# Kernel tuning notes

Measured on AMD Instinct MI355X. Metric: run time of the kernel, lower is better.

Reference implementation:

```python
import jax, jax.numpy as jnp
import numpy as np

TEMPERATURE = 8.0  # sqrt(head_dim=64)
_MASKING_VALUE = -1e30  # float32 branch of the original module


def setup_inputs() -> dict:
    key = jax.random.key(0)
    kq, kk, kv = jax.random.split(key, 3)
    B, H, S, D = 2, 12, 2048, 64
    q = jax.random.normal(kq, (B, H, S, D), dtype=jnp.float32)
    k = jax.random.normal(kk, (B, H, S, D), dtype=jnp.float32)
    v = jax.random.normal(kv, (B, H, S, D), dtype=jnp.float32)
    # causal mask, broadcastable over batch and heads; mask==0 -> masked
    mask = jnp.tril(jnp.ones((S, S), dtype=jnp.bool_))[None, None, :, :]
    return {"q": q, "k": k, "v": v, "mask": mask}


def reference(q, k, v, mask):
    # attn = (q / temperature) @ k^T  -> [B,H,S,S]
    scores = jnp.einsum("bhqd,bhkd->bhqk", q / TEMPERATURE, k)
    scores = jnp.where(mask, scores, _MASKING_VALUE)
    attn = jax.nn.softmax(scores, axis=-1)  # dropout in eval mode (identity)
    output = jnp.einsum("bhqk,bhkd->bhqd", attn, v)
    return (output, attn)
```

## Files before the change

kernel.cpp:

```cpp
#include <hip/hip_runtime.h>
#include <hip/hip_bf16.h>
#include <stdint.h>

#define SS 2048
#define DD 64
#define NHEAD 24
#define TK 64
#define NKT 32

typedef __attribute__((ext_vector_type(8))) short short8;
typedef __attribute__((ext_vector_type(4))) short short4v;
typedef __attribute__((ext_vector_type(4))) float f32x4;

#define QSCALE 0.18033688011112042f
#define MLOG   46.166241308446828f

#if __has_builtin(__builtin_amdgcn_exp2f)
#define EXP2(x) __builtin_amdgcn_exp2f(x)
#else
#define EXP2(x) exp2f(x)
#endif

__device__ __forceinline__ unsigned short f2bf(float x) {
  union { float f; unsigned u; } a; a.f = x;
  unsigned r = a.u + 0x7FFFu + ((a.u >> 16) & 1u);
  return (unsigned short)(r >> 16);
}

__device__ __forceinline__ void stage16(const unsigned char* g, unsigned char* l) {
  __builtin_amdgcn_global_load_lds(
      (const __attribute__((address_space(1))) unsigned int*)g,
      (__attribute__((address_space(3))) unsigned int*)l, 16, 0, 0);
}

__global__ __launch_bounds__(256) void prep_kernel(
    const float* __restrict__ q, const float* __restrict__ k,
    const float* __restrict__ v, unsigned short* __restrict__ qb,
    unsigned char* __restrict__ kb, unsigned char* __restrict__ vtb) {
  const int head = blockIdx.x >> 5;
  const int t64 = blockIdx.x & 31;
  const int tid = threadIdx.x;
  const int c4 = tid & 15;
  const size_t inbase = ((size_t)head * SS + (size_t)t64 * 64) * DD;
  const f32x4* qsrc = (const f32x4*)(q + inbase);
  const f32x4* ksrc = (const f32x4*)(k + inbase);
  const f32x4* vsrc = (const f32x4*)(v + inbase);
  unsigned short* qdst = qb + inbase;
  unsigned char* ktile = kb + ((size_t)(head * NKT + t64) << 13);
  unsigned char* vtile = vtb + ((size_t)(head * NKT + t64) << 13);
#pragma unroll
  for (int j = 0; j < 4; ++j) {
    const int row = (tid >> 4) + 16 * j;
    f32x4 xq = qsrc[row * 16 + c4];
    short4v hq;
    hq.x = (short)f2bf(xq.x * QSCALE); hq.y = (short)f2bf(xq.y * QSCALE);
    hq.z = (short)f2bf(xq.z * QSCALE); hq.w = (short)f2bf(xq.w * QSCALE);
    *(short4v*)(qdst + row * 64 + c4 * 4) = hq;

    f32x4 xk = ksrc[row * 16 + c4];
    short4v hk;
    hk.x = (short)f2bf(xk.x); hk.y = (short)f2bf(xk.y);
    hk.z = (short)f2bf(xk.z); hk.w = (short)f2bf(xk.w);
    const int chunk = c4 >> 1, half = c4 & 1;
    *(short4v*)(ktile + row * 128 + ((chunk ^ (row & 7)) << 4) + half * 8) = hk;

    f32x4 xv = vsrc[row * 16 + c4];
    float vals[4] = {xv.x, xv.y, xv.z, xv.w};
#pragma unroll
    for (int e = 0; e < 4; ++e) {
      const int d = c4 * 4 + e;
      *(unsigned short*)(vtile + d * 128 + (((row >> 3) ^ (d & 7)) << 4) +
                         (row & 7) * 2) = f2bf(vals[e]);
    }
  }
}

__global__ __launch_bounds__(256) void sdpa_kernel(
    const unsigned short* __restrict__ qb, const unsigned char* __restrict__ kb,
    const unsigned char* __restrict__ vtb, float* __restrict__ out,
    float* __restrict__ attn) {
  __shared__ unsigned char lds[32768];

  const int bid = blockIdx.x;
  const int xcd = bid & 7;
  const int seq = bid >> 3;
  const int head = xcd * 3 + (seq >> 5);
  const int qt = seq & 31;
  const int q0 = qt * TK;

  const int tid = threadIdx.x;
  const int w = tid >> 6;
  const int l = tid & 63;
  const int lhi = l >> 4;
  const int llo = l & 15;
  const int qrl = 16 * w + llo;

  const unsigned short* qh = qb + (size_t)head * SS * DD;
  const unsigned char* kh = kb + ((size_t)(head * NKT) << 13);
  const unsigned char* vh = vtb + ((size_t)(head * NKT) << 13);
  float* oh = out + (size_t)head * SS * DD;
  float* ah = attn + (size_t)head * SS * SS;
  float* ah_row = ah + (size_t)(q0 + qrl) * SS;

  short8 qf0 = *(const short8*)(qh + (size_t)(q0 + qrl) * DD + lhi * 8);
  short8 qf1 = *(const short8*)(qh + (size_t)(q0 + qrl) * DD + lhi * 8 + 32);

  float lsum = 0.f;
  stage16(kh + tid * 16, lds + tid * 16);
  stage16(kh + 4096 + tid * 16, lds + 4096 + tid * 16);
  __syncthreads();
  int b = 0;
  for (int kt = 0; kt <= qt; ++kt) {
    if (kt < qt) {
      const unsigned char* src = kh + ((size_t)(kt + 1) << 13);
      unsigned char* dst = lds + (b ^ 1) * 8192;
      stage16(src + tid * 16, dst + tid * 16);
      stage16(src + 4096 + tid * 16, dst + 4096 + tid * 16);
    }
    const unsigned char* kbuf = lds + b * 8192;
    const bool diag = (kt == qt);
#pragma unroll
    for (int c = 0; c < 4; ++c) {
      const int br = 16 * c + llo;
      short8 kf0 = *(const short8*)(kbuf + br * 128 + ((lhi ^ (br & 7)) << 4));
      short8 kf1 = *(const short8*)(kbuf + br * 128 + (((lhi + 4) ^ (br & 7)) << 4));
      f32x4 acc = {0.f, 0.f, 0.f, 0.f};
      acc = __builtin_amdgcn_mfma_f32_16x16x32_bf16(kf0, qf0, acc, 0, 0, 0);
      acc = __builtin_amdgcn_mfma_f32_16x16x32_bf16(kf1, qf1, acc, 0, 0, 0);
#pragma unroll
      for (int r = 0; r < 4; ++r) {
        float sv = acc[r];
        if (diag && (16 * c + 4 * lhi + r > qrl)) sv = -INFINITY;
        lsum += EXP2(sv - MLOG);
      }
    }
    __syncthreads();
    b ^= 1;
  }
  lsum += __shfl_xor(lsum, 16);
  lsum += __shfl_xor(lsum, 32);
  const float linv = 1.0f / lsum;

  f32x4 o[4];
#pragma unroll
  for (int c = 0; c < 4; ++c) o[c] = (f32x4){0.f, 0.f, 0.f, 0.f};

  unsigned sv[8];
  int k0p = 0;

  b = 0;
  stage16(kh + tid * 16, lds + tid * 16);
  stage16(kh + 4096 + tid * 16, lds + 4096 + tid * 16);
  stage16(vh + tid * 16, lds + 16384 + tid * 16);
  stage16(vh + 4096 + tid * 16, lds + 16384 + 4096 + tid * 16);
  __syncthreads();

  const int i0 = ((((2 * lhi)) & 3) * 16 + llo) * 4;
  const int i1 = ((((2 * lhi) + 1) & 3) * 16 + llo) * 4;

  for (int kt = 0; kt <= qt; ++kt) {
    if (kt > 0) {
#pragma unroll
      for (int c = 0; c < 4; ++c) {
        f32x4 fo;
        fo.x = __uint_as_float(sv[2 * c] << 16);
        fo.y = __uint_as_float(sv[2 * c] & 0xFFFF0000u);
        fo.z = __uint_as_float(sv[2 * c + 1] << 16);
        fo.w = __uint_as_float(sv[2 * c + 1] & 0xFFFF0000u);
        __builtin_nontemporal_store(fo, (f32x4*)(ah_row + k0p + 16 * c + 4 * lhi));
      }
    }
    if (kt < qt) {
      const unsigned char* ksrc = kh + ((size_t)(kt + 1) << 13);
      const unsigned char* vsrc = vh + ((size_t)(kt + 1) << 13);
      unsigned char* kdst = lds + (b ^ 1) * 8192;
      unsigned char* vdst = lds + 16384 + (b ^ 1) * 8192;
      stage16(ksrc + tid * 16, kdst + tid * 16);
      stage16(ksrc + 4096 + tid * 16, kdst + 4096 + tid * 16);
      stage16(vsrc + tid * 16, vdst + tid * 16);
      stage16(vsrc + 4096 + tid * 16, vdst + 4096 + tid * 16);
    }
    const unsigned char* kbuf = lds + b * 8192;
    const unsigned char* vbuf = lds + 16384 + b * 8192;
    const bool diag = (kt == qt);

    unsigned pk[8];
#pragma unroll
    for (int c = 0; c < 4; ++c) {
      const int br = 16 * c + llo;
      short8 kf0 = *(const short8*)(kbuf + br * 128 + ((lhi ^ (br & 7)) << 4));
      short8 kf1 = *(const short8*)(kbuf + br * 128 + (((lhi + 4) ^ (br & 7)) << 4));
      f32x4 acc = {0.f, 0.f, 0.f, 0.f};
      acc = __builtin_amdgcn_mfma_f32_16x16x32_bf16(kf0, qf0, acc, 0, 0, 0);
      acc = __builtin_amdgcn_mfma_f32_16x16x32_bf16(kf1, qf1, acc, 0, 0, 0);
      float p[4];
#pragma unroll
      for (int r = 0; r < 4; ++r) {
        float s = acc[r];
        if (diag && (16 * c + 4 * lhi + r > qrl)) s = -INFINITY;
        p[r] = EXP2(s - MLOG) * linv;
      }
      pk[2 * c] = ((unsigned)f2bf(p[1]) << 16) | f2bf(p[0]);
      pk[2 * c + 1] = ((unsigned)f2bf(p[3]) << 16) | f2bf(p[2]);
    }

    union U { int i[4]; short8 v; } fa0, fa1;
#pragma unroll
    for (int jb = 0; jb < 2; ++jb) {
      int a0 = __builtin_amdgcn_ds_bpermute(i0, (int)pk[0 + jb]);
      int b0 = __builtin_amdgcn_ds_bpermute(i0, (int)pk[2 + jb]);
      fa0.i[jb] = (lhi < 2) ? a0 : b0;
      int a1 = __builtin_amdgcn_ds_bpermute(i1, (int)pk[0 + jb]);
      int b1 = __builtin_amdgcn_ds_bpermute(i1, (int)pk[2 + jb]);
      fa0.i[2 + jb] = (lhi < 2) ? a1 : b1;
      int c0 = __builtin_amdgcn_ds_bpermute(i0, (int)pk[4 + jb]);
      int d0 = __builtin_amdgcn_ds_bpermute(i0, (int)pk[6 + jb]);
      fa1.i[jb] = (lhi < 2) ? c0 : d0;
      int c1 = __builtin_amdgcn_ds_bpermute(i1, (int)pk[4 + jb]);
      int d1 = __builtin_amdgcn_ds_bpermute(i1, (int)pk[6 + jb]);
      fa1.i[2 + jb] = (lhi < 2) ? c1 : d1;
    }

#pragma unroll
    for (int c = 0; c < 4; ++c) {
      const int vr = 16 * c + llo;
      short8 vb0 = *(const short8*)(vbuf + vr * 128 + ((lhi ^ (vr & 7)) << 4));
      short8 vb1 = *(const short8*)(vbuf + vr * 128 + (((lhi + 4) ^ (vr & 7)) << 4));
      o[c] = __builtin_amdgcn_mfma_f32_16x16x32_bf16(fa0.v, vb0, o[c], 0, 0, 0);
      o[c] = __builtin_amdgcn_mfma_f32_16x16x32_bf16(fa1.v, vb1, o[c], 0, 0, 0);
    }

#pragma unroll
    for (int t = 0; t < 8; ++t) sv[t] = pk[t];
    k0p = kt * TK;
    __syncthreads();
    b ^= 1;
  }
#pragma unroll
  for (int c = 0; c < 4; ++c) {
    f32x4 fo;
    fo.x = __uint_as_float(sv[2 * c] << 16);
    fo.y = __uint_as_float(sv[2 * c] & 0xFFFF0000u);
    fo.z = __uint_as_float(sv[2 * c + 1] << 16);
    fo.w = __uint_as_float(sv[2 * c + 1] & 0xFFFF0000u);
    __builtin_nontemporal_store(fo, (f32x4*)(ah_row + k0p + 16 * c + 4 * lhi));
  }

  {
    const int zc = (qt + 1) * TK;
#pragma unroll
    for (int j = 0; j < 4; ++j) {
      int row = q0 + 16 * w + 4 * j + lhi;
      f32x4* dst = (f32x4*)(ah + (size_t)row * SS);
      f32x4 z = {0.f, 0.f, 0.f, 0.f};
      for (int c = (zc >> 2) + llo; c < (SS >> 2); c += 16)
        __builtin_nontemporal_store(z, dst + c);
    }
  }

#pragma unroll
  for (int c = 0; c < 4; ++c)
#pragma unroll
    for (int r = 0; r < 4; ++r) {
      int qrow = q0 + 16 * w + 4 * lhi + r;
      oh[(size_t)qrow * DD + 16 * c + llo] = o[c][r];
    }
}

extern "C" void kernel_launch(void* const* d_in, const int* in_sizes, int n_in,
                              void* d_out, int out_size, void* d_ws, size_t ws_size,
                              hipStream_t stream) {
  const float* q = (const float*)d_in[0];
  const float* k = (const float*)d_in[1];
  const float* v = (const float*)d_in[2];
  float* out = (float*)d_out;
  float* attn = out + (size_t)NHEAD * SS * DD;

  const size_t QKV_BYTES = (size_t)NHEAD * SS * DD * 2;
  unsigned short* qb = (unsigned short*)d_ws;
  unsigned char* kb = (unsigned char*)d_ws + QKV_BYTES;
  unsigned char* vtb = kb + QKV_BYTES;

  prep_kernel<<<dim3(NHEAD * NKT), dim3(256), 0, stream>>>(q, k, v, qb, kb, vtb);
  sdpa_kernel<<<dim3(NHEAD * NKT), dim3(256), 0, stream>>>(qb, kb, vtb, out, attn);
}
```

Measured before the change: 516.5 us.

## Stage probabilities through LDS for coalesced attn stores and PV operands

P tiles are now written to an extra LDS buffer after softmax. They are read back once for row-coalesced full-width attn stores and once as MFMA A-operands, replacing the ds_bpermute shuffles and the per-lane scattered nontemporal stores. Normalization folds log2(lsum) into the exponent offset, removing one multiply per element. Query tiles are scheduled longest-first to balance the causal work, and the zero-fill uses regular rather than nontemporal stores. This adds an extra barrier per tile and 8KB of LDS, which may reduce occupancy.

```diff
diff --git a/kernel.cpp b/kernel.cpp
--- a/kernel.cpp
+++ b/kernel.cpp
@@ -21,10 +21,20 @@
 #define EXP2(x) exp2f(x)
 #endif
 
+#if __has_builtin(__builtin_amdgcn_logf)
+#define LOG2F(x) __builtin_amdgcn_logf(x)
+#else
+#define LOG2F(x) log2f(x)
+#endif
+
 __device__ __forceinline__ unsigned short f2bf(float x) {
   union { float f; unsigned u; } a; a.f = x;
   unsigned r = a.u + 0x7FFFu + ((a.u >> 16) & 1u);
   return (unsigned short)(r >> 16);
+}
+__device__ __forceinline__ float bf2f(unsigned short u) {
+  union { unsigned u; float f; } a; a.u = ((unsigned)u) << 16;
+  return a.f;
 }
 
 __device__ __forceinline__ void stage16(const unsigned char* g, unsigned char* l) {
@@ -79,13 +89,13 @@
     const unsigned short* __restrict__ qb, const unsigned char* __restrict__ kb,
     const unsigned char* __restrict__ vtb, float* __restrict__ out,
     float* __restrict__ attn) {
-  __shared__ unsigned char lds[32768];
+  __shared__ unsigned char lds[40960];
 
   const int bid = blockIdx.x;
   const int xcd = bid & 7;
   const int seq = bid >> 3;
   const int head = xcd * 3 + (seq >> 5);
-  const int qt = seq & 31;
+  const int qt = 31 - (seq & 31);
   const int q0 = qt * TK;
 
   const int tid = threadIdx.x;
@@ -100,7 +110,7 @@
   const unsigned char* vh = vtb + ((size_t)(head * NKT) << 13);
   float* oh = out + (size_t)head * SS * DD;
   float* ah = attn + (size_t)head * SS * SS;
-  float* ah_row = ah + (size_t)(q0 + qrl) * SS;
+  unsigned char* ldsP = lds + 32768;
 
   short8 qf0 = *(const short8*)(qh + (size_t)(q0 + qrl) * DD + lhi * 8);
   short8 qf1 = *(const short8*)(qh + (size_t)(q0 + qrl) * DD + lhi * 8 + 32);
@@ -139,14 +149,11 @@
   }
   lsum += __shfl_xor(lsum, 16);
   lsum += __shfl_xor(lsum, 32);
-  const float linv = 1.0f / lsum;
+  const float ladj = MLOG + LOG2F(lsum);
 
   f32x4 o[4];
 #pragma unroll
   for (int c = 0; c < 4; ++c) o[c] = (f32x4){0.f, 0.f, 0.f, 0.f};
-
-  unsigned sv[8];
-  int k0p = 0;
 
   b = 0;
   stage16(kh + tid * 16, lds + tid * 16);
@@ -155,21 +162,7 @@
   stage16(vh + 4096 + tid * 16, lds + 16384 + 4096 + tid * 16);
   __syncthreads();
 
-  const int i0 = ((((2 * lhi)) & 3) * 16 + llo) * 4;
-  const int i1 = ((((2 * lhi) + 1) & 3) * 16 + llo) * 4;
-
   for (int kt = 0; kt <= qt; ++kt) {
-    if (kt > 0) {
-#pragma unroll
-      for (int c = 0; c < 4; ++c) {
-        f32x4 fo;
-        fo.x = __uint_as_float(sv[2 * c] << 16);
-        fo.y = __uint_as_float(sv[2 * c] & 0xFFFF0000u);
-        fo.z = __uint_as_float(sv[2 * c + 1] << 16);
-        fo.w = __uint_as_float(sv[2 * c + 1] & 0xFFFF0000u);
-        __builtin_nontemporal_store(fo, (f32x4*)(ah_row + k0p + 16 * c + 4 * lhi));
-      }
-    }
     if (kt < qt) {
       const unsigned char* ksrc = kh + ((size_t)(kt + 1) << 13);
       const unsigned char* vsrc = vh + ((size_t)(kt + 1) << 13);
@@ -184,7 +177,6 @@
     const unsigned char* vbuf = lds + 16384 + b * 8192;
     const bool diag = (kt == qt);
 
-    unsigned pk[8];
 #pragma unroll
     for (int c = 0; c < 4; ++c) {
       const int br = 16 * c + llo;
@@ -198,63 +190,62 @@
       for (int r = 0; r < 4; ++r) {
         float s = acc[r];
         if (diag && (16 * c + 4 * lhi + r > qrl)) s = -INFINITY;
-        p[r] = EXP2(s - MLOG) * linv;
-      }
-      pk[2 * c] = ((unsigned)f2bf(p[1]) << 16) | f2bf(p[0]);
-      pk[2 * c + 1] = ((unsigned)f2bf(p[3]) << 16) | f2bf(p[2]);
-    }
-
-    union U { int i[4]; short8 v; } fa0, fa1;
-#pragma unroll
-    for (int jb = 0; jb < 2; ++jb) {
-      int a0 = __builtin_amdgcn_ds_bpermute(i0, (int)pk[0 + jb]);
-      int b0 = __builtin_amdgcn_ds_bpermute(i0, (int)pk[2 + jb]);
-      fa0.i[jb] = (lhi < 2) ? a0 : b0;
-      int a1 = __builtin_amdgcn_ds_bpermute(i1, (int)pk[0 + jb]);
-      int b1 = __builtin_amdgcn_ds_bpermute(i1, (int)pk[2 + jb]);
-      fa0.i[2 + jb] = (lhi < 2) ? a1 : b1;
-      int c0 = __builtin_amdgcn_ds_bpermute(i0, (int)pk[4 + jb]);
-      int d0 = __builtin_amdgcn_ds_bpermute(i0, (int)pk[6 + jb]);
-      fa1.i[jb] = (lhi < 2) ? c0 : d0;
-      int c1 = __builtin_amdgcn_ds_bpermute(i1, (int)pk[4 + jb]);
-      int d1 = __builtin_amdgcn_ds_bpermute(i1, (int)pk[6 + jb]);
-      fa1.i[2 + jb] = (lhi < 2) ? c1 : d1;
-    }
-
-#pragma unroll
-    for (int c = 0; c < 4; ++c) {
-      const int vr = 16 * c + llo;
-      short8 vb0 = *(const short8*)(vbuf + vr * 128 + ((lhi ^ (vr & 7)) << 4));
-      short8 vb1 = *(const short8*)(vbuf + vr * 128 + (((lhi + 4) ^ (vr & 7)) << 4));
-      o[c] = __builtin_amdgcn_mfma_f32_16x16x32_bf16(fa0.v, vb0, o[c], 0, 0, 0);
-      o[c] = __builtin_amdgcn_mfma_f32_16x16x32_bf16(fa1.v, vb1, o[c], 0, 0, 0);
-    }
-
-#pragma unroll
-    for (int t = 0; t < 8; ++t) sv[t] = pk[t];
-    k0p = kt * TK;
+        p[r] = EXP2(s - ladj);
+      }
+      short4v hv;
+      hv.x = (short)f2bf(p[0]); hv.y = (short)f2bf(p[1]);
+      hv.z = (short)f2bf(p[2]); hv.w = (short)f2bf(p[3]);
+      const int cc = 2 * c + (lhi >> 1);
+      *(short4v*)(ldsP + qrl * 128 + ((cc ^ (qrl & 7)) << 4) + ((lhi & 1) << 3)) = hv;
+    }
+
+    asm volatile("s_waitcnt lgkmcnt(0)" ::: "memory");
+    __builtin_amdgcn_s_barrier();
+    __builtin_amdgcn_sched_barrier(0);
+
+    {
+      const int k0 = kt * TK;
+      const int ro_b = (tid >> 4);
+      const int cg = tid & 15;
+#pragma unroll
+      for (int j = 0; j < 4; ++j) {
+        const int row = ro_b + 16 * j;
+        short4v pv = *(const short4v*)(ldsP + row * 128 +
+                                       (((cg >> 1) ^ (row & 7)) << 4) + ((cg & 1) << 3));
+        f32x4 fo;
+        fo.x = bf2f((unsigned short)pv.x);
+        fo.y = bf2f((unsigned short)pv.y);
+        fo.z = bf2f((unsigned short)pv.z);
+        fo.w = bf2f((unsigned short)pv.w);
+        *(f32x4*)(ah + (size_t)(q0 + row) * SS + k0 + cg * 4) = fo;
+      }
+    }
+
+    {
+      const int pr = 16 * w + llo;
+      short8 pa0 = *(const short8*)(ldsP + pr * 128 + ((lhi ^ (pr & 7)) << 4));
+      short8 pa1 = *(const short8*)(ldsP + pr * 128 + (((4 + lhi) ^ (pr & 7)) << 4));
+#pragma unroll
+      for (int c = 0; c < 4; ++c) {
+        const int vr = 16 * c + llo;
+        short8 vb0 = *(const short8*)(vbuf + vr * 128 + ((lhi ^ (vr & 7)) << 4));
+        short8 vb1 = *(const short8*)(vbuf + vr * 128 + (((lhi + 4) ^ (vr & 7)) << 4));
+        o[c] = __builtin_amdgcn_mfma_f32_16x16x32_bf16(pa0, vb0, o[c], 0, 0, 0);
+        o[c] = __builtin_amdgcn_mfma_f32_16x16x32_bf16(pa1, vb1, o[c], 0, 0, 0);
+      }
+    }
     __syncthreads();
     b ^= 1;
   }
-#pragma unroll
-  for (int c = 0; c < 4; ++c) {
-    f32x4 fo;
-    fo.x = __uint_as_float(sv[2 * c] << 16);
-    fo.y = __uint_as_float(sv[2 * c] & 0xFFFF0000u);
-    fo.z = __uint_as_float(sv[2 * c + 1] << 16);
-    fo.w = __uint_as_float(sv[2 * c + 1] & 0xFFFF0000u);
-    __builtin_nontemporal_store(fo, (f32x4*)(ah_row + k0p + 16 * c + 4 * lhi));
-  }
 
   {
     const int zc = (qt + 1) * TK;
+    f32x4 z = {0.f, 0.f, 0.f, 0.f};
 #pragma unroll
     for (int j = 0; j < 4; ++j) {
       int row = q0 + 16 * w + 4 * j + lhi;
       f32x4* dst = (f32x4*)(ah + (size_t)row * SS);
-      f32x4 z = {0.f, 0.f, 0.f, 0.f};
-      for (int c = (zc >> 2) + llo; c < (SS >> 2); c += 16)
-        __builtin_nontemporal_store(z, dst + c);
+      for (int c = (zc >> 2) + llo; c < (SS >> 2); c += 16) dst[c] = z;
     }
   }
 
```

Measured after the change: 476.5 us. 1.08x faster.
